# Performance work log

Measured on AMD Instinct MI355X. Metric: run time of the kernel, lower is better.

Reference implementation:

```python
import jax, jax.numpy as jnp
import numpy as np

B, P, N, E, H, KD, M = 64, 100, 1000, 512, 8, 64, 10
SQRT_E = float(np.sqrt(E))
CLIP = 10.0


def _heads(x):
    # [b, n, H*KD] -> [b, H, n, KD]
    b, n, _ = x.shape
    return x.reshape(b, n, H, KD).transpose(0, 2, 1, 3)


def setup_inputs() -> dict:
    key = jax.random.key(0)
    ks = jax.random.split(key, 20)
    f = jnp.float32
    s = 0.02  # weight init scale
    return {
        "encoded_last_node": jax.random.normal(ks[0], (B, P, E), f),
        "encoded_last_agents": jax.random.normal(ks[1], (B, P, E), f),
        "cur_dist": jax.random.uniform(ks[2], (B, P, N), f, 1e-3, 1.0),
        "ninf_mask": jnp.zeros((B, P, N), f),
        "lengths": jax.random.uniform(ks[3], (B, P, M), f),
        "max_dis": jax.random.uniform(ks[4], (B, P, 1), f),
        "remain_max_dis": jax.random.uniform(ks[5], (B, P, 1), f),
        "q_first": 0.5 * jax.random.normal(ks[6], (B, H, P, KD), f),
        "k": 0.5 * jax.random.normal(ks[7], (B, H, N, KD), f),
        "v": 0.5 * jax.random.normal(ks[8], (B, H, N, KD), f),
        "single_head_key": 0.5 * jax.random.normal(ks[9], (B, E, N), f),
        "Wq_last_w": s * jax.random.normal(ks[10], (H * KD, 2 * E + 2), f),
        "dis_emb_w": s * jax.random.normal(ks[11], (H * KD, 4), f),
        "mh_w": s * jax.random.normal(ks[12], (E, H * KD), f),
        "mh_b": s * jax.random.normal(ks[13], (E,), f),
        "dist_alpha": jnp.ones((1,), f),
        "depot_num": jax.random.randint(ks[14], (B,), 1, M + 1),
        "route_cnt": jax.random.randint(ks[15], (B, P, 1), 0, M),
        "left_city": jax.random.randint(ks[16], (B, P), 0, N + 1),
        "city_num": N,
    }


def reference(encoded_last_node, encoded_last_agents, cur_dist, ninf_mask,
              lengths, max_dis, remain_max_dis, q_first, k, v, single_head_key,
              Wq_last_w, dis_emb_w, mh_w, mh_b, dist_alpha,
              depot_num, route_cnt, left_city, city_num):
    # route_num = depot_num - 1, broadcast to route_cnt shape [B,P,1]
    route_num = jnp.broadcast_to(depot_num[:, None, None], route_cnt.shape) - 1
    g_cur = jnp.take_along_axis(lengths, route_cnt, axis=-1)    # [B,P,1]
    g_route = jnp.take_along_axis(lengths, route_num, axis=-1)  # [B,P,1]
    q_info_in = jnp.concatenate([g_cur, g_route, max_dis, remain_max_dis], axis=-1)  # [B,P,4]
    q_info = _heads(q_info_in @ dis_emb_w.T)  # [B,H,P,KD]

    frac = 1.0 - (route_cnt + 1).astype(jnp.float32) / (route_num + 1).astype(jnp.float32)
    lc = left_city[:, :, None].astype(jnp.float32) / city_num
    q_last_in = jnp.concatenate([encoded_last_node, encoded_last_agents, frac, lc], axis=-1)  # [B,P,2E+2]
    q_last = _heads(q_last_in @ Wq_last_w.T)  # [B,H,P,KD]

    q = q_first + q_last + q_info  # [B,H,P,KD]

    # masked multi-head attention (rank3 ninf mask)
    score = jnp.einsum("bhpd,bhnd->bhpn", q, k) / jnp.sqrt(jnp.float32(KD))
    score = score + ninf_mask[:, None, :, :]
    w = jax.nn.softmax(score, axis=-1)
    out = jnp.einsum("bhpn,bhnd->bhpd", w, v)
    out_concat = out.transpose(0, 2, 1, 3).reshape(out.shape[0], out.shape[2], H * KD)  # [B,P,H*KD]
    mh = out_concat @ mh_w.T + mh_b  # [B,P,E]

    # single-head distance-biased scoring
    score2 = jnp.einsum("bpe,ben->bpn", mh, single_head_key)  # [B,P,N]
    max_dist = jnp.max(cur_dist, axis=-1, keepdims=True)
    cur_dist_out = -cur_dist / max_dist
    score_clipped = CLIP * jnp.tanh(score2 / SQRT_E + dist_alpha * cur_dist_out)
    probs = jax.nn.softmax(score_clipped + ninf_mask, axis=-1)
    return probs
```

## Files before the change

kernel.cpp:

```cpp
#include <hip/hip_runtime.h>
#include <hip/hip_bf16.h>

#define BB 64
#define PP 100
#define NN 1000
#define EE 512
#define HH 8
#define KDD 64
#define MM 10
#define ROWS (BB*PP)
#define K1K 1026
#define INVSQE 0.044194173824159216f
#define CLIPV 10.0f

union F4 { float4 v; float f[4]; };

using bf16x8 = __attribute__((ext_vector_type(8))) short;
using bf16x4 = __attribute__((ext_vector_type(4))) unsigned short;
using f32x4  = __attribute__((ext_vector_type(4))) float;

__device__ inline unsigned short f2bf(float x) {
  unsigned u = __float_as_uint(x);
  u += 0x7FFFu + ((u >> 16) & 1u);
  return (unsigned short)(u >> 16);
}

__device__ inline float bf2f(unsigned short s) {
  return __uint_as_float(((unsigned)s) << 16);
}

__device__ inline float fast_tanh(float x) {
  float e = __expf(2.0f * x);
  return 1.0f - 2.0f / (e + 1.0f);
}

__global__ __launch_bounds__(256) void k_rowmax(const float* __restrict__ cd,
                                                float* __restrict__ rmax) {
  int row = blockIdx.x * 4 + (threadIdx.x >> 6);
  int lane = threadIdx.x & 63;
  const float* src = cd + (size_t)row * NN;
  float m = -1e30f;
  for (int i = lane; i < NN; i += 64) m = fmaxf(m, src[i]);
  #pragma unroll
  for (int off = 32; off; off >>= 1) m = fmaxf(m, __shfl_xor(m, off));
  if (lane == 0) rmax[row] = m;
}

__global__ __launch_bounds__(256) void k_qgemm(
    const float* __restrict__ eln, const float* __restrict__ ela,
    const float* __restrict__ lengths, const float* __restrict__ max_dis,
    const float* __restrict__ remain, const float* __restrict__ q_first,
    const float* __restrict__ Wq, const float* __restrict__ dis_emb,
    const int* __restrict__ depot, const int* __restrict__ route_cnt,
    const int* __restrict__ left_city, const int* __restrict__ city_num,
    float* __restrict__ qout) {
  __shared__ unsigned short Xs[64][40];
  __shared__ unsigned short Ws[64][40];
  __shared__ float info_s[64][4];
  __shared__ float fl_s[64][2];
  const int t = threadIdx.x;
  const int lane = t & 63;
  const int w = t >> 6;
  const int lr = lane & 15, lg = lane >> 4;
  const int rowBase = blockIdx.y * 64, colBase = blockIdx.x * 64;

  if (t < 64) {
    int row = rowBase + t;
    int b = row / PP;
    int rc = route_cnt[row];
    int rn = depot[b] - 1;
    info_s[t][0] = lengths[row * MM + rc];
    info_s[t][1] = lengths[row * MM + rn];
    info_s[t][2] = max_dis[row];
    info_s[t][3] = remain[row];
    fl_s[t][0] = 1.0f - (float)(rc + 1) / (float)(rn + 1);
    fl_s[t][1] = (float)left_city[row] / (float)city_num[0];
  }

  f32x4 acc[4];
  #pragma unroll
  for (int m = 0; m < 4; ++m) { acc[m][0] = 0.f; acc[m][1] = 0.f; acc[m][2] = 0.f; acc[m][3] = 0.f; }

  for (int kt = 0; kt < 32; ++kt) {
    const float* xsrc = (kt < 16) ? eln : ela;
    const int koff = (kt & 15) * 32;
    __syncthreads();
    #pragma unroll
    for (int i = 0; i < 2; ++i) {
      int s = i * 256 + t;
      int r = s >> 3, c4 = (s & 7) * 4;
      F4 xv, wv;
      xv.v = *(const float4*)&xsrc[(size_t)(rowBase + r) * 512 + koff + c4];
      wv.v = *(const float4*)&Wq[(size_t)(colBase + r) * K1K + kt * 32 + c4];
      unsigned short* xd = &Xs[r][c4];
      unsigned short* wd = &Ws[r][c4];
      xd[0] = f2bf(xv.f[0]); xd[1] = f2bf(xv.f[1]); xd[2] = f2bf(xv.f[2]); xd[3] = f2bf(xv.f[3]);
      wd[0] = f2bf(wv.f[0]); wd[1] = f2bf(wv.f[1]); wd[2] = f2bf(wv.f[2]); wd[3] = f2bf(wv.f[3]);
    }
    __syncthreads();
    bf16x8 bfr = *(bf16x8*)&Ws[w * 16 + lr][lg * 8];
    #pragma unroll
    for (int m = 0; m < 4; ++m) {
      bf16x8 af = *(bf16x8*)&Xs[m * 16 + lr][lg * 8];
      acc[m] = __builtin_amdgcn_mfma_f32_16x16x32_bf16(af, bfr, acc[m], 0, 0, 0);
    }
  }

  const int o = colBase + w * 16 + lr;
  F4 de; de.v = *(const float4*)&dis_emb[(size_t)o * 4];
  const float wq1024 = Wq[(size_t)o * K1K + 1024];
  const float wq1025 = Wq[(size_t)o * K1K + 1025];
  const int h = o >> 6, kd = o & 63;
  #pragma unroll
  for (int m = 0; m < 4; ++m) {
    #pragma unroll
    for (int j = 0; j < 4; ++j) {
      int r = m * 16 + lg * 4 + j;
      int row = rowBase + r;
      int b = row / PP, p = row % PP;
      F4 inf; inf.v = *(const float4*)&info_s[r][0];
      float v = acc[m][j]
              + inf.f[0] * de.f[0] + inf.f[1] * de.f[1]
              + inf.f[2] * de.f[2] + inf.f[3] * de.f[3]
              + fl_s[r][0] * wq1024 + fl_s[r][1] * wq1025
              + q_first[(((size_t)b * HH + h) * PP + p) * KDD + kd];
      qout[(size_t)row * 512 + o] = v;
    }
  }
}

__global__ __launch_bounds__(256) void k_attn(
    const float* __restrict__ qin, const float* __restrict__ kk,
    const float* __restrict__ vv, const float* __restrict__ mask,
    float* __restrict__ attn_out) {
  __shared__ unsigned short Kl[64][72];
  __shared__ unsigned short Vt[64][72];
  __shared__ unsigned short Pb[64][72];

  const int t = threadIdx.x;
  const int lane = t & 63;
  const int w = t >> 6;
  const int lr = lane & 15, lg = lane >> 4;
  const int gid = blockIdx.x;
  const int b = gid & 63;
  const int X = gid >> 6;
  const int h = X & 7, half = X >> 3;
  const int bh = b * HH + h;
  const int p0 = half * 64;
  const int nrows = (half == 0) ? 64 : (PP - 64);
  const bool active = (w * 16 < nrows);

  #pragma unroll
  for (int i = 0; i < 4; ++i) {
    int idx = i * 256 + t;
    int r = idx >> 4, c4 = (idx & 15) * 4;
    int p = p0 + r;
    F4 qv; qv.v = make_float4(0.f, 0.f, 0.f, 0.f);
    if (p < PP) qv.v = *(const float4*)&qin[((size_t)(b * PP + p)) * 512 + h * 64 + c4];
    bf16x4 pk;
    pk[0] = f2bf(qv.f[0] * 0.125f); pk[1] = f2bf(qv.f[1] * 0.125f);
    pk[2] = f2bf(qv.f[2] * 0.125f); pk[3] = f2bf(qv.f[3] * 0.125f);
    *(bf16x4*)&Pb[r][c4] = pk;
  }
  __syncthreads();

  bf16x8 qf[2];
  qf[0] = *(bf16x8*)&Pb[w * 16 + lr][lg * 8];
  qf[1] = *(bf16x8*)&Pb[w * 16 + lr][32 + lg * 8];

  float Lacc[4] = {0.f, 0.f, 0.f, 0.f};
  f32x4 Oa[4];
  #pragma unroll
  for (int dt = 0; dt < 4; ++dt) { Oa[dt][0] = 0.f; Oa[dt][1] = 0.f; Oa[dt][2] = 0.f; Oa[dt][3] = 0.f; }

  F4 kreg[4], vreg[4];
  const int vb2 = t & 15, va = t >> 4;

  #pragma unroll
  for (int i = 0; i < 4; ++i) {
    int idx = i * 256 + t;
    int r = idx >> 4, c4 = (idx & 15) * 4;
    kreg[i].v = (r < NN) ? *(const float4*)&kk[(((size_t)bh * NN) + r) * 64 + c4]
                         : make_float4(0.f, 0.f, 0.f, 0.f);
  }
  #pragma unroll
  for (int r = 0; r < 4; ++r) {
    int n = 4 * vb2 + r;
    vreg[r].v = (n < NN) ? *(const float4*)&vv[(((size_t)bh * NN) + n) * 64 + 4 * va]
                         : make_float4(0.f, 0.f, 0.f, 0.f);
  }

  for (int ch = 0; ch < 16; ++ch) {
    const int n0 = ch * 64;
    __syncthreads();

    #pragma unroll
    for (int i = 0; i < 4; ++i) {
      int idx = i * 256 + t;
      int r = idx >> 4, c4 = (idx & 15) * 4;
      bf16x4 pk;
      pk[0] = f2bf(kreg[i].f[0]); pk[1] = f2bf(kreg[i].f[1]);
      pk[2] = f2bf(kreg[i].f[2]); pk[3] = f2bf(kreg[i].f[3]);
      *(bf16x4*)&Kl[r][c4] = pk;
    }
    #pragma unroll
    for (int c = 0; c < 4; ++c) {
      bf16x4 pv;
      pv[0] = f2bf(vreg[0].f[c]); pv[1] = f2bf(vreg[1].f[c]);
      pv[2] = f2bf(vreg[2].f[c]); pv[3] = f2bf(vreg[3].f[c]);
      *(bf16x4*)&Vt[4 * va + c][4 * vb2] = pv;
    }
    __syncthreads();

    if (ch + 1 < 16) {
      const int nn0 = n0 + 64;
      #pragma unroll
      for (int i = 0; i < 4; ++i) {
        int idx = i * 256 + t;
        int r = idx >> 4, c4 = (idx & 15) * 4;
        int n = nn0 + r;
        kreg[i].v = (n < NN) ? *(const float4*)&kk[(((size_t)bh * NN) + n) * 64 + c4]
                             : make_float4(0.f, 0.f, 0.f, 0.f);
      }
      #pragma unroll
      for (int r = 0; r < 4; ++r) {
        int n = nn0 + 4 * vb2 + r;
        vreg[r].v = (n < NN) ? *(const float4*)&vv[(((size_t)bh * NN) + n) * 64 + 4 * va]
                             : make_float4(0.f, 0.f, 0.f, 0.f);
      }
    }

    if (active) {
      float ml[4][4];
      #pragma unroll
      for (int j = 0; j < 4; ++j) {
        int p = p0 + w * 16 + lg * 4 + j;
        #pragma unroll
        for (int nb = 0; nb < 4; ++nb) {
          int n = n0 + nb * 16 + lr;
          ml[j][nb] = (p < PP && n < NN) ? mask[((size_t)(b * PP + p)) * NN + n] : -1e30f;
        }
      }
      f32x4 sa[4];
      #pragma unroll
      for (int nb = 0; nb < 4; ++nb) { sa[nb][0] = 0.f; sa[nb][1] = 0.f; sa[nb][2] = 0.f; sa[nb][3] = 0.f; }
      #pragma unroll
      for (int kb = 0; kb < 2; ++kb)
        #pragma unroll
        for (int nb = 0; nb < 4; ++nb) {
          bf16x8 kf = *(bf16x8*)&Kl[nb * 16 + lr][kb * 32 + lg * 8];
          sa[nb] = __builtin_amdgcn_mfma_f32_16x16x32_bf16(qf[kb], kf, sa[nb], 0, 0, 0);
        }
      #pragma unroll
      for (int j = 0; j < 4; ++j) {
        int pr = w * 16 + lg * 4 + j;
        #pragma unroll
        for (int nb = 0; nb < 4; ++nb) {
          float e = __expf(sa[nb][j] + ml[j][nb]);
          Lacc[j] += e;
          Pb[pr][nb * 16 + lr] = f2bf(e);
        }
      }
      #pragma unroll
      for (int kb = 0; kb < 2; ++kb) {
        bf16x8 pf = *(bf16x8*)&Pb[w * 16 + lr][kb * 32 + lg * 8];
        #pragma unroll
        for (int dt = 0; dt < 4; ++dt) {
          bf16x8 vf = *(bf16x8*)&Vt[dt * 16 + lr][kb * 32 + lg * 8];
          Oa[dt] = __builtin_amdgcn_mfma_f32_16x16x32_bf16(pf, vf, Oa[dt], 0, 0, 0);
        }
      }
    }
  }

  if (active) {
    #pragma unroll
    for (int j = 0; j < 4; ++j) {
      float L = Lacc[j];
      #pragma unroll
      for (int off = 1; off < 16; off <<= 1) L += __shfl_xor(L, off);
      int p = p0 + w * 16 + lg * 4 + j;
      if (p < PP) {
        float inv = (L > 0.f) ? 1.0f / L : 0.f;
        #pragma unroll
        for (int dt = 0; dt < 4; ++dt)
          attn_out[((size_t)(b * PP + p)) * 512 + h * 64 + dt * 16 + lr] = Oa[dt][j] * inv;
      }
    }
  }
}

__global__ __launch_bounds__(256) void k_mhgemm(
    const float* __restrict__ A, const float* __restrict__ W,
    const float* __restrict__ bias, float* __restrict__ out) {
  __shared__ unsigned short Xs[64][40];
  __shared__ unsigned short Ws[64][40];
  const int t = threadIdx.x;
  const int lane = t & 63;
  const int w = t >> 6;
  const int lr = lane & 15, lg = lane >> 4;
  const int rowBase = blockIdx.y * 64, colBase = blockIdx.x * 64;

  f32x4 acc[4];
  #pragma unroll
  for (int m = 0; m < 4; ++m) { acc[m][0] = 0.f; acc[m][1] = 0.f; acc[m][2] = 0.f; acc[m][3] = 0.f; }

  for (int kt = 0; kt < 16; ++kt) {
    const int koff = kt * 32;
    __syncthreads();
    #pragma unroll
    for (int i = 0; i < 2; ++i) {
      int s = i * 256 + t;
      int r = s >> 3, c4 = (s & 7) * 4;
      F4 xv, wv;
      xv.v = *(const float4*)&A[(size_t)(rowBase + r) * 512 + koff + c4];
      wv.v = *(const float4*)&W[(size_t)(colBase + r) * 512 + koff + c4];
      unsigned short* xd = &Xs[r][c4];
      unsigned short* wd = &Ws[r][c4];
      xd[0] = f2bf(xv.f[0]); xd[1] = f2bf(xv.f[1]); xd[2] = f2bf(xv.f[2]); xd[3] = f2bf(xv.f[3]);
      wd[0] = f2bf(wv.f[0]); wd[1] = f2bf(wv.f[1]); wd[2] = f2bf(wv.f[2]); wd[3] = f2bf(wv.f[3]);
    }
    __syncthreads();
    bf16x8 bfr = *(bf16x8*)&Ws[w * 16 + lr][lg * 8];
    #pragma unroll
    for (int m = 0; m < 4; ++m) {
      bf16x8 af = *(bf16x8*)&Xs[m * 16 + lr][lg * 8];
      acc[m] = __builtin_amdgcn_mfma_f32_16x16x32_bf16(af, bfr, acc[m], 0, 0, 0);
    }
  }

  const int o = colBase + w * 16 + lr;
  const float bv = bias[o];
  #pragma unroll
  for (int m = 0; m < 4; ++m) {
    #pragma unroll
    for (int j = 0; j < 4; ++j) {
      int row = rowBase + m * 16 + lg * 4 + j;
      out[(size_t)row * 512 + o] = acc[m][j] + bv;
    }
  }
}

__global__ __launch_bounds__(256) void k_final_score(
    const float* __restrict__ mh, const float* __restrict__ shk,
    const float* __restrict__ cur_dist, const float* __restrict__ rmax,
    const float* __restrict__ mask, const float* __restrict__ dist_alpha,
    float* __restrict__ sc_out) {
  __shared__ unsigned short As[112][40];
  __shared__ unsigned short Bt[64][40];
  const int t = threadIdx.x;
  const int lane = t & 63;
  const int w = t >> 6;
  const int lr = lane & 15, lg = lane >> 4;
  const int n0 = blockIdx.x * 64, b = blockIdx.y;

  f32x4 acc[7];
  #pragma unroll
  for (int m = 0; m < 7; ++m) { acc[m][0] = 0.f; acc[m][1] = 0.f; acc[m][2] = 0.f; acc[m][3] = 0.f; }

  for (int kt = 0; kt < 16; ++kt) {
    const int k0 = kt * 32;
    __syncthreads();
    #pragma unroll
    for (int i = 0; i < 4; ++i) {
      int s = i * 256 + t;
      if (s < 896) {
        int r = s >> 3, c4 = (s & 7) * 4;
        F4 xv; xv.v = make_float4(0.f, 0.f, 0.f, 0.f);
        if (r < PP) xv.v = *(const float4*)&mh[(size_t)(b * PP + r) * 512 + k0 + c4];
        unsigned short* xd = &As[r][c4];
        xd[0] = f2bf(xv.f[0]); xd[1] = f2bf(xv.f[1]); xd[2] = f2bf(xv.f[2]); xd[3] = f2bf(xv.f[3]);
      }
    }
    if (t < 128) {
      int a = t & 15, kb = t >> 4;
      F4 rowv[4];
      #pragma unroll
      for (int r = 0; r < 4; ++r) {
        int k = k0 + 4 * kb + r;
        int n = n0 + 4 * a;
        rowv[r].v = (n < NN) ? *(const float4*)&shk[((size_t)b * EE + k) * NN + n]
                             : make_float4(0.f, 0.f, 0.f, 0.f);
      }
      #pragma unroll
      for (int c = 0; c < 4; ++c) {
        unsigned short* dst = &Bt[4 * a + c][4 * kb];
        dst[0] = f2bf(rowv[0].f[c]); dst[1] = f2bf(rowv[1].f[c]);
        dst[2] = f2bf(rowv[2].f[c]); dst[3] = f2bf(rowv[3].f[c]);
      }
    }
    __syncthreads();
    bf16x8 bfr = *(bf16x8*)&Bt[w * 16 + lr][lg * 8];
    #pragma unroll
    for (int m = 0; m < 7; ++m) {
      bf16x8 af = *(bf16x8*)&As[m * 16 + lr][lg * 8];
      acc[m] = __builtin_amdgcn_mfma_f32_16x16x32_bf16(af, bfr, acc[m], 0, 0, 0);
    }
  }

  const float alpha = dist_alpha[0];
  const int n = n0 + w * 16 + lr;
  if (n < NN) {
    #pragma unroll
    for (int m = 0; m < 7; ++m) {
      #pragma unroll
      for (int j = 0; j < 4; ++j) {
        int p = m * 16 + lg * 4 + j;
        if (p >= PP) continue;
        size_t rb = (size_t)(b * PP + p) * NN;
        float rmx = rmax[b * PP + p];
        float cd = cur_dist[rb + n];
        float mk = mask[rb + n];
        sc_out[rb + n] = CLIPV * fast_tanh(acc[m][j] * INVSQE - alpha * cd / rmx) + mk;
      }
    }
  }
}

__global__ __launch_bounds__(256) void k_softmax(const float* __restrict__ sc,
                                                 float* __restrict__ out) {
  __shared__ float redm[4];
  __shared__ float redsum[4];
  const int row = blockIdx.x;
  const int t = threadIdx.x;
  const float* src = sc + (size_t)row * NN;
  float v0[4];
  float m = -1e30f;
  #pragma unroll
  for (int i = 0; i < 4; ++i) {
    int n = i * 256 + t;
    v0[i] = (n < NN) ? src[n] : -1e30f;
    m = fmaxf(m, v0[i]);
  }
  #pragma unroll
  for (int off = 32; off; off >>= 1) m = fmaxf(m, __shfl_xor(m, off));
  int wid = t >> 6, lane = t & 63;
  if (lane == 0) redm[wid] = m;
  __syncthreads();
  m = fmaxf(fmaxf(redm[0], redm[1]), fmaxf(redm[2], redm[3]));
  float e[4];
  float s = 0.f;
  #pragma unroll
  for (int i = 0; i < 4; ++i) {
    int n = i * 256 + t;
    e[i] = (n < NN) ? __expf(v0[i] - m) : 0.f;
    s += e[i];
  }
  #pragma unroll
  for (int off = 32; off; off >>= 1) s += __shfl_xor(s, off);
  if (lane == 0) redsum[wid] = s;
  __syncthreads();
  s = redsum[0] + redsum[1] + redsum[2] + redsum[3];
  float inv = 1.0f / s;
  #pragma unroll
  for (int i = 0; i < 4; ++i) {
    int n = i * 256 + t;
    if (n < NN) out[(size_t)row * NN + n] = e[i] * inv;
  }
}

extern "C" void kernel_launch(void* const* d_in, const int* in_sizes, int n_in,
                              void* d_out, int out_size, void* d_ws, size_t ws_size,
                              hipStream_t stream) {
  const float* eln       = (const float*)d_in[0];
  const float* ela       = (const float*)d_in[1];
  const float* cur_dist  = (const float*)d_in[2];
  const float* ninf      = (const float*)d_in[3];
  const float* lengths   = (const float*)d_in[4];
  const float* max_dis   = (const float*)d_in[5];
  const float* remain    = (const float*)d_in[6];
  const float* q_first   = (const float*)d_in[7];
  const float* kten      = (const float*)d_in[8];
  const float* vten      = (const float*)d_in[9];
  const float* shk       = (const float*)d_in[10];
  const float* Wq        = (const float*)d_in[11];
  const float* dis_emb   = (const float*)d_in[12];
  const float* mh_w      = (const float*)d_in[13];
  const float* mh_b      = (const float*)d_in[14];
  const float* dalpha    = (const float*)d_in[15];
  const int*   depot     = (const int*)d_in[16];
  const int*   route_cnt = (const int*)d_in[17];
  const int*   left_city = (const int*)d_in[18];
  const int*   city_num  = (const int*)d_in[19];
  float* out = (float*)d_out;

  float* ws      = (float*)d_ws;
  float* q_ws    = ws;
  float* attn_ws = q_ws + (size_t)ROWS * 512;
  float* mh_ws   = attn_ws + (size_t)ROWS * 512;
  float* sc_ws   = mh_ws + (size_t)ROWS * 512;
  float* rmax_ws = sc_ws + (size_t)ROWS * NN;

  k_rowmax<<<ROWS / 4, 256, 0, stream>>>(cur_dist, rmax_ws);
  k_qgemm<<<dim3(8, 100), 256, 0, stream>>>(eln, ela, lengths, max_dis, remain,
                                            q_first, Wq, dis_emb, depot, route_cnt,
                                            left_city, city_num, q_ws);
  k_attn<<<1024, 256, 0, stream>>>(q_ws, kten, vten, ninf, attn_ws);
  k_mhgemm<<<dim3(8, 100), 256, 0, stream>>>(attn_ws, mh_w, mh_b, mh_ws);
  k_final_score<<<dim3(16, 64), 256, 0, stream>>>(mh_ws, shk, cur_dist, rmax_ws,
                                                  ninf, dalpha, sc_ws);
  k_softmax<<<ROWS, 256, 0, stream>>>(sc_ws, out);
}
```

Before: 285.4 us.

## Double-buffer K/V register prefetch and stage mask through shared memory as bf16

```diff
diff --git a/kernel.cpp b/kernel.cpp
--- a/kernel.cpp
+++ b/kernel.cpp
@@ -20,9 +20,10 @@
 using f32x4  = __attribute__((ext_vector_type(4))) float;
 
 __device__ inline unsigned short f2bf(float x) {
-  unsigned u = __float_as_uint(x);
-  u += 0x7FFFu + ((u >> 16) & 1u);
-  return (unsigned short)(u >> 16);
+  __hip_bfloat16 h = __float2bfloat16(x);
+  unsigned short u;
+  __builtin_memcpy(&u, &h, sizeof(u));
+  return u;
 }
 
 __device__ inline float bf2f(unsigned short s) {
@@ -135,7 +136,7 @@
     float* __restrict__ attn_out) {
   __shared__ unsigned short Kl[64][72];
   __shared__ unsigned short Vt[64][72];
-  __shared__ unsigned short Pb[64][72];
+  __shared__ unsigned short PMb[64][72];
 
   const int t = threadIdx.x;
   const int lane = t & 63;
@@ -149,6 +150,30 @@
   const int p0 = half * 64;
   const int nrows = (half == 0) ? 64 : (PP - 64);
   const bool active = (w * 16 < nrows);
+  const int vb2 = t & 15, va = t >> 4;
+
+  F4 kA[4], vA[4], kB[4], vB[4];
+
+  auto loadKV = [&](F4 (&kreg)[4], F4 (&vreg)[4], int ch) {
+    const int n0 = ch * 64;
+    #pragma unroll
+    for (int i = 0; i < 4; ++i) {
+      int idx = i * 256 + t;
+      int r = idx >> 4, c4 = (idx & 15) * 4;
+      int n = n0 + r;
+      kreg[i].v = (n < NN) ? *(const float4*)&kk[(((size_t)bh * NN) + n) * 64 + c4]
+                           : make_float4(0.f, 0.f, 0.f, 0.f);
+    }
+    #pragma unroll
+    for (int r = 0; r < 4; ++r) {
+      int n = n0 + 4 * vb2 + r;
+      vreg[r].v = (n < NN) ? *(const float4*)&vv[(((size_t)bh * NN) + n) * 64 + 4 * va]
+                           : make_float4(0.f, 0.f, 0.f, 0.f);
+    }
+  };
+
+  loadKV(kA, vA, 0);
+  loadKV(kB, vB, 1);
 
   #pragma unroll
   for (int i = 0; i < 4; ++i) {
@@ -160,40 +185,39 @@
     bf16x4 pk;
     pk[0] = f2bf(qv.f[0] * 0.125f); pk[1] = f2bf(qv.f[1] * 0.125f);
     pk[2] = f2bf(qv.f[2] * 0.125f); pk[3] = f2bf(qv.f[3] * 0.125f);
-    *(bf16x4*)&Pb[r][c4] = pk;
+    *(bf16x4*)&PMb[r][c4] = pk;
   }
   __syncthreads();
 
   bf16x8 qf[2];
-  qf[0] = *(bf16x8*)&Pb[w * 16 + lr][lg * 8];
-  qf[1] = *(bf16x8*)&Pb[w * 16 + lr][32 + lg * 8];
+  qf[0] = *(bf16x8*)&PMb[w * 16 + lr][lg * 8];
+  qf[1] = *(bf16x8*)&PMb[w * 16 + lr][32 + lg * 8];
 
   float Lacc[4] = {0.f, 0.f, 0.f, 0.f};
   f32x4 Oa[4];
   #pragma unroll
   for (int dt = 0; dt < 4; ++dt) { Oa[dt][0] = 0.f; Oa[dt][1] = 0.f; Oa[dt][2] = 0.f; Oa[dt][3] = 0.f; }
 
-  F4 kreg[4], vreg[4];
-  const int vb2 = t & 15, va = t >> 4;
-
-  #pragma unroll
-  for (int i = 0; i < 4; ++i) {
-    int idx = i * 256 + t;
-    int r = idx >> 4, c4 = (idx & 15) * 4;
-    kreg[i].v = (r < NN) ? *(const float4*)&kk[(((size_t)bh * NN) + r) * 64 + c4]
-                         : make_float4(0.f, 0.f, 0.f, 0.f);
-  }
-  #pragma unroll
-  for (int r = 0; r < 4; ++r) {
-    int n = 4 * vb2 + r;
-    vreg[r].v = (n < NN) ? *(const float4*)&vv[(((size_t)bh * NN) + n) * 64 + 4 * va]
-                         : make_float4(0.f, 0.f, 0.f, 0.f);
-  }
-
-  for (int ch = 0; ch < 16; ++ch) {
+  auto chunk_step = [&](F4 (&kreg)[4], F4 (&vreg)[4], int ch) {
     const int n0 = ch * 64;
     __syncthreads();
 
+    F4 mload[4];
+    #pragma unroll
+    for (int i = 0; i < 4; ++i) {
+      int idx = i * 256 + t;
+      int r = idx >> 4, c4 = (idx & 15) * 4;
+      if (r < nrows) {
+        int p = p0 + r, n = n0 + c4;
+        if (n + 3 < NN) {
+          mload[i].v = *(const float4*)&mask[((size_t)(b * PP + p)) * NN + n];
+        } else {
+          #pragma unroll
+          for (int j = 0; j < 4; ++j)
+            mload[i].f[j] = (n + j < NN) ? mask[((size_t)(b * PP + p)) * NN + n + j] : -1e30f;
+        }
+      }
+    }
     #pragma unroll
     for (int i = 0; i < 4; ++i) {
       int idx = i * 256 + t;
@@ -210,37 +234,22 @@
       pv[2] = f2bf(vreg[2].f[c]); pv[3] = f2bf(vreg[3].f[c]);
       *(bf16x4*)&Vt[4 * va + c][4 * vb2] = pv;
     }
-    __syncthreads();
-
-    if (ch + 1 < 16) {
-      const int nn0 = n0 + 64;
-      #pragma unroll
-      for (int i = 0; i < 4; ++i) {
-        int idx = i * 256 + t;
-        int r = idx >> 4, c4 = (idx & 15) * 4;
-        int n = nn0 + r;
-        kreg[i].v = (n < NN) ? *(const float4*)&kk[(((size_t)bh * NN) + n) * 64 + c4]
-                             : make_float4(0.f, 0.f, 0.f, 0.f);
-      }
-      #pragma unroll
-      for (int r = 0; r < 4; ++r) {
-        int n = nn0 + 4 * vb2 + r;
-        vreg[r].v = (n < NN) ? *(const float4*)&vv[(((size_t)bh * NN) + n) * 64 + 4 * va]
-                             : make_float4(0.f, 0.f, 0.f, 0.f);
-      }
-    }
+    #pragma unroll
+    for (int i = 0; i < 4; ++i) {
+      int idx = i * 256 + t;
+      int r = idx >> 4, c4 = (idx & 15) * 4;
+      if (r < nrows) {
+        bf16x4 pk;
+        pk[0] = f2bf(mload[i].f[0]); pk[1] = f2bf(mload[i].f[1]);
+        pk[2] = f2bf(mload[i].f[2]); pk[3] = f2bf(mload[i].f[3]);
+        *(bf16x4*)&PMb[r][c4] = pk;
+      }
+    }
+    __syncthreads();
+
+    if (ch + 2 < 16) loadKV(kreg, vreg, ch + 2);
 
     if (active) {
-      float ml[4][4];
-      #pragma unroll
-      for (int j = 0; j < 4; ++j) {
-        int p = p0 + w * 16 + lg * 4 + j;
-        #pragma unroll
-        for (int nb = 0; nb < 4; ++nb) {
-          int n = n0 + nb * 16 + lr;
-          ml[j][nb] = (p < PP && n < NN) ? mask[((size_t)(b * PP + p)) * NN + n] : -1e30f;
-        }
-      }
       f32x4 sa[4];
       #pragma unroll
       for (int nb = 0; nb < 4; ++nb) { sa[nb][0] = 0.f; sa[nb][1] = 0.f; sa[nb][2] = 0.f; sa[nb][3] = 0.f; }
@@ -256,14 +265,15 @@
         int pr = w * 16 + lg * 4 + j;
         #pragma unroll
         for (int nb = 0; nb < 4; ++nb) {
-          float e = __expf(sa[nb][j] + ml[j][nb]);
+          float mv = bf2f(PMb[pr][nb * 16 + lr]);
+          float e = __expf(sa[nb][j] + mv);
           Lacc[j] += e;
-          Pb[pr][nb * 16 + lr] = f2bf(e);
+          PMb[pr][nb * 16 + lr] = f2bf(e);
         }
       }
       #pragma unroll
       for (int kb = 0; kb < 2; ++kb) {
-        bf16x8 pf = *(bf16x8*)&Pb[w * 16 + lr][kb * 32 + lg * 8];
+        bf16x8 pf = *(bf16x8*)&PMb[w * 16 + lr][kb * 32 + lg * 8];
         #pragma unroll
         for (int dt = 0; dt < 4; ++dt) {
           bf16x8 vf = *(bf16x8*)&Vt[dt * 16 + lr][kb * 32 + lg * 8];
@@ -271,6 +281,12 @@
         }
       }
     }
+  };
+
+  #pragma unroll 1
+  for (int cc = 0; cc < 8; ++cc) {
+    chunk_step(kA, vA, 2 * cc);
+    chunk_step(kB, vB, 2 * cc + 1);
   }
 
   if (active) {
```

Result: slower. 318.0 us (+11.4%).
